# Kernel tuning notes

Hardware: AMD Instinct MI355X
Metric: run time of the kernel (lower is better)

Reference implementation:

```python
import jax, jax.numpy as jnp
import numpy as np

B, DIM, GRID, K, H = 524288, 4, 16, 100, 512
FEAT = DIM + 1 + K  # 105


def setup_inputs() -> dict:
    key = jax.random.key(0)
    ks = jax.random.split(key, 16)
    s = 0.05
    return {
        "x": jax.random.uniform(ks[0], (B, DIM), dtype=jnp.float32),
        "min_values": jnp.zeros((DIM,), jnp.float32),
        "max_values": jnp.ones((DIM,), jnp.float32),
        "pivots": jax.random.uniform(ks[1], (GRID ** DIM, DIM), dtype=jnp.float32),
        "knnd": jax.random.uniform(ks[2], (GRID ** DIM, K), dtype=jnp.float32),
        "query_mean": 0.1 * jax.random.normal(ks[3], (DIM,), jnp.float32),
        "query_std": 0.5 + jax.random.uniform(ks[4], (DIM,), dtype=jnp.float32),
        "knnd_mean": 0.1 * jax.random.normal(ks[5], (K,), jnp.float32),
        "knnd_std": 0.5 + jax.random.uniform(ks[6], (K,), dtype=jnp.float32),
        "W1": s * jax.random.normal(ks[7], (FEAT, H), jnp.float32),
        "b1": jnp.zeros((H,), jnp.float32),
        "W2": s * jax.random.normal(ks[8], (H, H), jnp.float32),
        "b2": jnp.zeros((H,), jnp.float32),
        "W3": s * jax.random.normal(ks[9], (H, H), jnp.float32),
        "b3": jnp.zeros((H,), jnp.float32),
        "W4": s * jax.random.normal(ks[10], (H, K), jnp.float32),
        "b4": jnp.zeros((K,), jnp.float32),
    }


def reference(x, min_values, max_values, pivots, knnd,
              query_mean, query_std, knnd_mean, knnd_std,
              W1, b1, W2, b2, W3, b3, W4, b4):
    dim = x.shape[1]
    grid = GRID
    bin_width = (max_values - min_values) / grid            # [dim]
    cell_diag = jnp.sqrt(jnp.sum(bin_width ** 2))
    # grid-hash index (radix base `grid` over dims)
    scaled = (x - min_values) / (max_values - min_values) * grid
    bins = jnp.clip(jnp.floor(scaled).astype(jnp.int32), 0, grid - 1)  # [B,dim]
    radix = (grid ** jnp.arange(dim - 1, -1, -1)).astype(jnp.int32)    # [dim]
    idx = jnp.sum(bins * radix, axis=-1)                    # [B]
    # gather pivot coords + knn distances
    pivot = pivots[idx]                                     # [B,dim]
    pknnd = knnd[idx]                                       # [B,K]
    dist = jnp.linalg.norm(x - pivot, axis=-1) / cell_diag  # [B]
    # normalize feature parts
    qn = (x - query_mean) / query_std                       # [B,dim]
    kn = (pknnd - knnd_mean) / knnd_std                     # [B,K]
    feat = jnp.concatenate([qn, dist[:, None], kn], axis=-1)  # [B,105]
    # 4-layer MLP
    h = jax.nn.relu(feat @ W1 + b1)
    h = jax.nn.relu(h @ W2 + b2)
    h = jax.nn.relu(h @ W3 + b3)
    return h @ W4 + b4
```

## Files before the change

### kernel.cpp

```cpp
#include <hip/hip_runtime.h>

typedef __attribute__((ext_vector_type(8))) short short8_t;
typedef __attribute__((ext_vector_type(16))) float f32x16;

#define NROWS_TOTAL 524288
#define MROWS 128
#define HSTRIDE 536
#define NTHREADS 512
#define OSTRIDE 108

__device__ __forceinline__ unsigned short f32_to_bf16(float f) {
    union { float f; unsigned int u; } v; v.f = f;
    unsigned int r = v.u + 0x7FFFu + ((v.u >> 16) & 1u);
    return (unsigned short)(r >> 16);
}

__global__ void conv_weights(const float* __restrict__ W1, const float* __restrict__ W2,
                             const float* __restrict__ W3, const float* __restrict__ W4,
                             unsigned short* __restrict__ ws) {
    int i = blockIdx.x * 256 + threadIdx.x;
    if (i < 65536) {
        int k = i & 127, n = i >> 7;
        ws[i] = f32_to_bf16(k < 105 ? W1[k * 512 + n] : 0.0f);
    } else if (i < 327680) {
        int j = i - 65536; int k = j & 511, n = j >> 9;
        ws[i] = f32_to_bf16(W2[k * 512 + n]);
    } else if (i < 589824) {
        int j = i - 327680; int k = j & 511, n = j >> 9;
        ws[i] = f32_to_bf16(W3[k * 512 + n]);
    } else if (i < 655360) {
        int j = i - 589824; int k = j & 511, n = j >> 9;
        ws[i] = f32_to_bf16(n < 100 ? W4[k * 100 + n] : 0.0f);
    }
}

__device__ __forceinline__ int clamp_bin(float sc) {
    int b = (int)floorf(sc);
    return b < 0 ? 0 : (b > 15 ? 15 : b);
}

template<int KDIM>
__device__ __forceinline__ void mlp_layer(unsigned short* hbuf,
                                          const unsigned short* __restrict__ Wt,
                                          const float* __restrict__ bias,
                                          int lane, int wave) {
    const int l31 = lane & 31;
    const int lh  = lane >> 5;
    const int n0  = wave * 64;
    constexpr int NK = KDIM / 32;

    f32x16 acc[4][2];
    #pragma unroll
    for (int nt = 0; nt < 2; ++nt) {
        float bv = bias[n0 + nt * 32 + l31];
        #pragma unroll
        for (int mt = 0; mt < 4; ++mt)
            #pragma unroll
            for (int r = 0; r < 16; ++r)
                acc[mt][nt][r] = bv;
    }

    const unsigned short* wbase  = Wt + (n0 + l31) * KDIM + lh * 8;
    const unsigned short* abase0 = hbuf + l31 * HSTRIDE + lh * 8;

    short8_t bc[2][4];
    #pragma unroll
    for (int nt = 0; nt < 2; ++nt)
        #pragma unroll
        for (int kh = 0; kh < 2; ++kh) {
            bc[0][nt * 2 + kh] = *(const short8_t*)(wbase + nt * (32 * KDIM) + kh * 16);
            bc[1][nt * 2 + kh] = *(const short8_t*)(wbase + nt * (32 * KDIM) + 32 + kh * 16);
        }

    #pragma unroll
    for (int kc = 0; kc < NK; ++kc) {
        const int par = kc & 1;
        short8_t a[4][2];
        #pragma unroll
        for (int mt = 0; mt < 4; ++mt)
            #pragma unroll
            for (int kh = 0; kh < 2; ++kh)
                a[mt][kh] = *(const short8_t*)(abase0 + mt * (32 * HSTRIDE) + kc * 32 + kh * 16);
        __builtin_amdgcn_s_setprio(1);
        #pragma unroll
        for (int kh = 0; kh < 2; ++kh)
            #pragma unroll
            for (int mt = 0; mt < 4; ++mt)
                #pragma unroll
                for (int nt = 0; nt < 2; ++nt)
                    acc[mt][nt] = __builtin_amdgcn_mfma_f32_32x32x16_bf16(
                        a[mt][kh], bc[par][nt * 2 + kh], acc[mt][nt], 0, 0, 0);
        __builtin_amdgcn_s_setprio(0);
        if (kc + 2 < NK) {
            #pragma unroll
            for (int nt = 0; nt < 2; ++nt)
                #pragma unroll
                for (int kh = 0; kh < 2; ++kh)
                    bc[par][nt * 2 + kh] =
                        *(const short8_t*)(wbase + nt * (32 * KDIM) + (kc + 2) * 32 + kh * 16);
        }
    }

    __syncthreads();

    const int odd = lane & 1;
    const int colw = n0 + odd * 32 + (l31 & ~1);
    #pragma unroll
    for (int mt = 0; mt < 4; ++mt) {
        #pragma unroll
        for (int reg = 0; reg < 16; ++reg) {
            float vA = fmaxf(acc[mt][0][reg], 0.f);
            float vB = fmaxf(acc[mt][1][reg], 0.f);
            float vm = odd ? vB : vA;
            float vs = odd ? vA : vB;
            float vr = __shfl_xor(vs, 1, 64);
            unsigned int ha = f32_to_bf16(vm);
            unsigned int hb = f32_to_bf16(vr);
            unsigned int packed = odd ? (hb | (ha << 16)) : (ha | (hb << 16));
            int row = mt * 32 + (reg & 3) + 8 * (reg >> 2) + 4 * lh;
            *(unsigned int*)(hbuf + row * HSTRIDE + colw) = packed;
        }
    }
    __syncthreads();
}

__global__ void __launch_bounds__(NTHREADS, 2)
pivnet_fused(const float* __restrict__ x,
             const float* __restrict__ minv, const float* __restrict__ maxv,
             const float* __restrict__ pivots, const float* __restrict__ knnd,
             const float* __restrict__ qmean, const float* __restrict__ qstd,
             const float* __restrict__ kmean, const float* __restrict__ kstd,
             const unsigned short* __restrict__ wsw,
             const float* __restrict__ b1, const float* __restrict__ b2,
             const float* __restrict__ b3, const float* __restrict__ b4,
             float* __restrict__ out) {
    __shared__ unsigned short hbuf[MROWS * HSTRIDE];

    const int tid  = threadIdx.x;
    const int lane = tid & 63;
    const int wave = tid >> 6;
    const int row0 = blockIdx.x * MROWS;

    {
        const int p = tid & 7;
        const float mn0 = minv[0], mn1 = minv[1], mn2 = minv[2], mn3 = minv[3];
        const float rg0 = maxv[0] - mn0, rg1 = maxv[1] - mn1, rg2 = maxv[2] - mn2, rg3 = maxv[3] - mn3;
        const float cd2 = (rg0 * rg0 + rg1 * rg1 + rg2 * rg2 + rg3 * rg3) * (1.0f / 256.0f);
        #pragma unroll
        for (int rep = 0; rep < 2; ++rep) {
            const int r = (tid >> 3) + rep * 64;
            const float4 xr = ((const float4*)x)[row0 + r];
            const float xa0 = xr.x, xa1 = xr.y, xa2 = xr.z, xa3 = xr.w;
            int bidx;
            bidx = clamp_bin((xa0 - mn0) / rg0 * 16.f);
            bidx = bidx * 16 + clamp_bin((xa1 - mn1) / rg1 * 16.f);
            bidx = bidx * 16 + clamp_bin((xa2 - mn2) / rg2 * 16.f);
            bidx = bidx * 16 + clamp_bin((xa3 - mn3) / rg3 * 16.f);
            const float* kr = knnd + (size_t)bidx * 100;

            unsigned short vals[16];
            if (p == 0) {
                vals[0] = f32_to_bf16((xa0 - qmean[0]) / qstd[0]);
                vals[1] = f32_to_bf16((xa1 - qmean[1]) / qstd[1]);
                vals[2] = f32_to_bf16((xa2 - qmean[2]) / qstd[2]);
                vals[3] = f32_to_bf16((xa3 - qmean[3]) / qstd[3]);
                const float4 pv = ((const float4*)pivots)[bidx];
                float d0 = xa0 - pv.x, d1 = xa1 - pv.y, d2 = xa2 - pv.z, d3 = xa3 - pv.w;
                vals[4] = f32_to_bf16(sqrtf((d0 * d0 + d1 * d1 + d2 * d2 + d3 * d3) / cd2));
                #pragma unroll
                for (int j = 5; j < 16; ++j) {
                    int k = j - 5;
                    vals[j] = f32_to_bf16((kr[k] - kmean[k]) / kstd[k]);
                }
            } else {
                #pragma unroll
                for (int j = 0; j < 16; ++j) {
                    int k = p * 16 + j - 5;
                    float f = 0.f;
                    if (k < 100) f = (kr[k] - kmean[k]) / kstd[k];
                    vals[j] = f32_to_bf16(f);
                }
            }
            unsigned int pk[8];
            #pragma unroll
            for (int j = 0; j < 8; ++j)
                pk[j] = (unsigned int)vals[2 * j] | ((unsigned int)vals[2 * j + 1] << 16);
            uint4* d4 = (uint4*)(hbuf + r * HSTRIDE + p * 16);
            d4[0] = make_uint4(pk[0], pk[1], pk[2], pk[3]);
            d4[1] = make_uint4(pk[4], pk[5], pk[6], pk[7]);
        }
    }
    __syncthreads();

    const unsigned short* W1t = wsw;
    const unsigned short* W2t = wsw + 65536;
    const unsigned short* W3t = wsw + 327680;
    const unsigned short* W4t = wsw + 589824;

    mlp_layer<128>(hbuf, W1t, b1, lane, wave);
    mlp_layer<512>(hbuf, W2t, b2, lane, wave);
    mlp_layer<512>(hbuf, W3t, b3, lane, wave);

    {
        const int l31 = lane & 31;
        const int lh  = lane >> 5;
        const int nt4  = wave & 3;
        const int rowg = wave >> 2;
        const int col  = nt4 * 32 + l31;
        f32x16 acc4[2];
        {
            float bv = (col < 100) ? b4[col] : 0.f;
            #pragma unroll
            for (int mt = 0; mt < 2; ++mt)
                #pragma unroll
                for (int r = 0; r < 16; ++r) acc4[mt][r] = bv;
        }
        const unsigned short* wb4 = W4t + col * 512 + lh * 8;
        const unsigned short* ab0 = hbuf + (rowg * 64 + l31) * HSTRIDE + lh * 8;

        short8_t b4c[2][2];
        #pragma unroll
        for (int kh = 0; kh < 2; ++kh) {
            b4c[0][kh] = *(const short8_t*)(wb4 + kh * 16);
            b4c[1][kh] = *(const short8_t*)(wb4 + 32 + kh * 16);
        }

        #pragma unroll
        for (int kc = 0; kc < 16; ++kc) {
            const int par = kc & 1;
            short8_t a[2][2];
            #pragma unroll
            for (int mt = 0; mt < 2; ++mt)
                #pragma unroll
                for (int kh = 0; kh < 2; ++kh)
                    a[mt][kh] = *(const short8_t*)(ab0 + mt * (32 * HSTRIDE) + kc * 32 + kh * 16);
            __builtin_amdgcn_s_setprio(1);
            #pragma unroll
            for (int kh = 0; kh < 2; ++kh)
                #pragma unroll
                for (int mt = 0; mt < 2; ++mt)
                    acc4[mt] = __builtin_amdgcn_mfma_f32_32x32x16_bf16(
                        a[mt][kh], b4c[par][kh], acc4[mt], 0, 0, 0);
            __builtin_amdgcn_s_setprio(0);
            if (kc + 2 < 16) {
                #pragma unroll
                for (int kh = 0; kh < 2; ++kh)
                    b4c[par][kh] = *(const short8_t*)(wb4 + (kc + 2) * 32 + kh * 16);
            }
        }

        __syncthreads();

        float* fstage = (float*)hbuf;
        if (col < 100) {
            #pragma unroll
            for (int mt = 0; mt < 2; ++mt)
                #pragma unroll
                for (int reg = 0; reg < 16; ++reg) {
                    int row = rowg * 64 + mt * 32 + (reg & 3) + 8 * (reg >> 2) + 4 * lh;
                    fstage[row * OSTRIDE + col] = acc4[mt][reg];
                }
        }
        __syncthreads();

        float* obase = out + (size_t)row0 * 100;
        #pragma unroll
        for (int k = 0; k < 7; ++k) {
            int j = tid + k * 512;
            if (j < 3200) {
                int row = j / 25;
                int c4  = j - row * 25;
                float4 v = *(const float4*)(fstage + row * OSTRIDE + c4 * 4);
                *(float4*)(obase + 4 * j) = v;
            }
        }
    }
}

extern "C" void kernel_launch(void* const* d_in, const int* in_sizes, int n_in,
                              void* d_out, int out_size, void* d_ws, size_t ws_size,
                              hipStream_t stream) {
    const float* x    = (const float*)d_in[0];
    const float* minv = (const float*)d_in[1];
    const float* maxv = (const float*)d_in[2];
    const float* piv  = (const float*)d_in[3];
    const float* knnd = (const float*)d_in[4];
    const float* qm   = (const float*)d_in[5];
    const float* qs   = (const float*)d_in[6];
    const float* km   = (const float*)d_in[7];
    const float* ks   = (const float*)d_in[8];
    const float* W1   = (const float*)d_in[9];
    const float* b1   = (const float*)d_in[10];
    const float* W2   = (const float*)d_in[11];
    const float* b2   = (const float*)d_in[12];
    const float* W3   = (const float*)d_in[13];
    const float* b3   = (const float*)d_in[14];
    const float* W4   = (const float*)d_in[15];
    const float* b4   = (const float*)d_in[16];
    float* out = (float*)d_out;
    unsigned short* wsw = (unsigned short*)d_ws;

    conv_weights<<<2560, 256, 0, stream>>>(W1, W2, W3, W4, wsw);
    pivnet_fused<<<NROWS_TOTAL / MROWS, NTHREADS, 0, stream>>>(
        x, minv, maxv, piv, knnd, qm, qs, km, ks,
        wsw, b1, b2, b3, b4, out);
}
```

Measured before the change: 1.290 ms.

## Stage weight tiles into LDS via async global_load_lds double buffering

Weights are repacked into k-chunked, XOR-swizzled tiles. Each block now streams them into a double-buffered LDS area with global_load_lds, gated by vmcnt waits and barriers, and the next layer's first tiles are prefetched while the current layer finishes. Before, every wave loaded its own weight fragments straight from global memory. Rows per block drop from 128 to 64 to make room for the staging buffers and to cut register use. The change trades per-wave global weight traffic for block-shared LDS reuse, at the cost of more barriers per k-step and less reuse of each weight tile per block.

```diff
diff --git a/kernel.cpp b/kernel.cpp
--- a/kernel.cpp
+++ b/kernel.cpp
@@ -4,10 +4,13 @@
 typedef __attribute__((ext_vector_type(16))) float f32x16;
 
 #define NROWS_TOTAL 524288
-#define MROWS 128
+#define MROWS 64
 #define HSTRIDE 536
 #define NTHREADS 512
 #define OSTRIDE 108
+
+#define HBUF_USHORT (MROWS * HSTRIDE)
+#define LDS_TOTAL_USHORT (HBUF_USHORT + 2 * 16384)
 
 __device__ __forceinline__ unsigned short f32_to_bf16(float f) {
     union { float f; unsigned int u; } v; v.f = f;
@@ -18,20 +21,16 @@
 __global__ void conv_weights(const float* __restrict__ W1, const float* __restrict__ W2,
                              const float* __restrict__ W3, const float* __restrict__ W4,
                              unsigned short* __restrict__ ws) {
-    int i = blockIdx.x * 256 + threadIdx.x;
-    if (i < 65536) {
-        int k = i & 127, n = i >> 7;
-        ws[i] = f32_to_bf16(k < 105 ? W1[k * 512 + n] : 0.0f);
-    } else if (i < 327680) {
-        int j = i - 65536; int k = j & 511, n = j >> 9;
-        ws[i] = f32_to_bf16(W2[k * 512 + n]);
-    } else if (i < 589824) {
-        int j = i - 327680; int k = j & 511, n = j >> 9;
-        ws[i] = f32_to_bf16(W3[k * 512 + n]);
-    } else if (i < 655360) {
-        int j = i - 589824; int k = j & 511, n = j >> 9;
-        ws[i] = f32_to_bf16(n < 100 ? W4[k * 100 + n] : 0.0f);
-    }
+    int t = blockIdx.x * 256 + threadIdx.x;
+    float v; int n, k, base;
+    if (t < 65536)       { n = t & 511;                 k = t >> 9;          v = (k < 105) ? W1[k * 512 + n] : 0.f; base = 0      + (k >> 5) * 16384; }
+    else if (t < 327680) { int u = t - 65536;  n = u & 511; k = u >> 9;      v = W2[k * 512 + n];                   base = 65536  + (k >> 5) * 16384; }
+    else if (t < 589824) { int u = t - 327680; n = u & 511; k = u >> 9;      v = W3[k * 512 + n];                   base = 327680 + (k >> 5) * 16384; }
+    else                 { int u = t - 589824; n = u & 127; k = u >> 7;      v = (n < 100) ? W4[k * 100 + n] : 0.f; base = 589824 + (k >> 5) * 4096;  }
+    int kk = k & 31;
+    int kh = kk >> 4, lh = (kk >> 3) & 1, i = kk & 7;
+    int off = (((n << 5) + (kh << 4) + (lh << 3)) ^ ((n & 7) << 3)) + i;
+    ws[base + off] = f32_to_bf16(v);
 }
 
 __device__ __forceinline__ int clamp_bin(float sc) {
@@ -39,74 +38,98 @@
     return b < 0 ? 0 : (b > 15 ? 15 : b);
 }
 
-template<int KDIM>
-__device__ __forceinline__ void mlp_layer(unsigned short* hbuf,
-                                          const unsigned short* __restrict__ Wt,
-                                          const float* __restrict__ bias,
-                                          int lane, int wave) {
-    const int l31 = lane & 31;
-    const int lh  = lane >> 5;
-    const int n0  = wave * 64;
+__device__ __forceinline__ void gl2lds16(const void* g, void* l) {
+    __builtin_amdgcn_global_load_lds(
+        (__attribute__((address_space(1))) void*)g,
+        (__attribute__((address_space(3))) void*)l, 16, 0, 0);
+}
+
+template<int CALLS>
+__device__ __forceinline__ void stageN(char* dst, const char* src, int tid) {
+    #pragma unroll
+    for (int c = 0; c < CALLS; ++c)
+        gl2lds16(src + c * 8192 + tid * 16, dst + c * 8192 + (tid >> 6) * 1024);
+}
+
+__device__ __forceinline__ void wait_vmcnt(int n) {
+    if (n == 0)      asm volatile("s_waitcnt vmcnt(0)" ::: "memory");
+    else if (n == 1) asm volatile("s_waitcnt vmcnt(1)" ::: "memory");
+    else             asm volatile("s_waitcnt vmcnt(4)" ::: "memory");
+}
+
+template<int KDIM, int NEXT_CALLS, int PREV_GATE>
+__device__ __forceinline__ void mlp_layer(unsigned short* hbuf, char* bst,
+                                          const unsigned short* Wt, const unsigned short* Wnext,
+                                          const float* __restrict__ bias, int tid) {
     constexpr int NK = KDIM / 32;
-
-    f32x16 acc[4][2];
+    const int lane = tid & 63, wave = tid >> 6;
+    const int l31 = lane & 31, lh = lane >> 5;
+    const int n0 = wave * 64;
+    const char* wt_b = (const char*)Wt;
+    const char* wn_b = (const char*)Wnext;
+
+    f32x16 acc[2][2];
     #pragma unroll
     for (int nt = 0; nt < 2; ++nt) {
         float bv = bias[n0 + nt * 32 + l31];
         #pragma unroll
-        for (int mt = 0; mt < 4; ++mt)
-            #pragma unroll
-            for (int r = 0; r < 16; ++r)
-                acc[mt][nt][r] = bv;
-    }
-
-    const unsigned short* wbase  = Wt + (n0 + l31) * KDIM + lh * 8;
-    const unsigned short* abase0 = hbuf + l31 * HSTRIDE + lh * 8;
-
-    short8_t bc[2][4];
+        for (int mt = 0; mt < 2; ++mt)
+            #pragma unroll
+            for (int r = 0; r < 16; ++r) acc[mt][nt][r] = bv;
+    }
+
+    const char* ab = (const char*)hbuf + l31 * (HSTRIDE * 2) + lh * 16;
+    int boff[2][2];
     #pragma unroll
     for (int nt = 0; nt < 2; ++nt)
         #pragma unroll
         for (int kh = 0; kh < 2; ++kh) {
-            bc[0][nt * 2 + kh] = *(const short8_t*)(wbase + nt * (32 * KDIM) + kh * 16);
-            bc[1][nt * 2 + kh] = *(const short8_t*)(wbase + nt * (32 * KDIM) + 32 + kh * 16);
+            int n = n0 + nt * 32 + l31;
+            boff[nt][kh] = ((n << 6) + (kh << 5) + (lh << 4)) ^ ((l31 & 7) << 4);
         }
 
     #pragma unroll
     for (int kc = 0; kc < NK; ++kc) {
-        const int par = kc & 1;
-        short8_t a[4][2];
-        #pragma unroll
-        for (int mt = 0; mt < 4; ++mt)
+        int gate = (kc == 0) ? PREV_GATE
+                 : ((kc + 1) < NK ? 4 : (((kc + 1 - NK) < 2 && NEXT_CALLS > 0) ? NEXT_CALLS : 0));
+        wait_vmcnt(gate);
+        __builtin_amdgcn_s_barrier();
+        const char* bp = bst + (kc & 1) * 32768;
+        short8_t b[2][2], a[2][2];
+        #pragma unroll
+        for (int nt = 0; nt < 2; ++nt)
             #pragma unroll
             for (int kh = 0; kh < 2; ++kh)
-                a[mt][kh] = *(const short8_t*)(abase0 + mt * (32 * HSTRIDE) + kc * 32 + kh * 16);
+                b[nt][kh] = *(const short8_t*)(bp + boff[nt][kh]);
+        #pragma unroll
+        for (int mt = 0; mt < 2; ++mt)
+            #pragma unroll
+            for (int kh = 0; kh < 2; ++kh)
+                a[mt][kh] = *(const short8_t*)(ab + mt * (32 * HSTRIDE * 2) + kc * 64 + kh * 32);
+        asm volatile("s_waitcnt lgkmcnt(0)" ::: "memory");
+        __builtin_amdgcn_sched_barrier(0);
+        __builtin_amdgcn_s_barrier();
+        char* mybuf = bst + (kc & 1) * 32768;
+        if (kc + 2 < NK)
+            stageN<4>(mybuf, wt_b + (kc + 2) * 32768, tid);
+        else if (NEXT_CALLS > 0 && (kc + 2 - NK) < 2)
+            stageN<NEXT_CALLS>(mybuf, wn_b + (kc + 2 - NK) * (NEXT_CALLS * 8192), tid);
         __builtin_amdgcn_s_setprio(1);
         #pragma unroll
         for (int kh = 0; kh < 2; ++kh)
             #pragma unroll
-            for (int mt = 0; mt < 4; ++mt)
+            for (int mt = 0; mt < 2; ++mt)
                 #pragma unroll
                 for (int nt = 0; nt < 2; ++nt)
                     acc[mt][nt] = __builtin_amdgcn_mfma_f32_32x32x16_bf16(
-                        a[mt][kh], bc[par][nt * 2 + kh], acc[mt][nt], 0, 0, 0);
+                        a[mt][kh], b[nt][kh], acc[mt][nt], 0, 0, 0);
         __builtin_amdgcn_s_setprio(0);
-        if (kc + 2 < NK) {
-            #pragma unroll
-            for (int nt = 0; nt < 2; ++nt)
-                #pragma unroll
-                for (int kh = 0; kh < 2; ++kh)
-                    bc[par][nt * 2 + kh] =
-                        *(const short8_t*)(wbase + nt * (32 * KDIM) + (kc + 2) * 32 + kh * 16);
-        }
-    }
-
-    __syncthreads();
+    }
 
     const int odd = lane & 1;
     const int colw = n0 + odd * 32 + (l31 & ~1);
     #pragma unroll
-    for (int mt = 0; mt < 4; ++mt) {
+    for (int mt = 0; mt < 2; ++mt) {
         #pragma unroll
         for (int reg = 0; reg < 16; ++reg) {
             float vA = fmaxf(acc[mt][0][reg], 0.f);
@@ -121,7 +144,8 @@
             *(unsigned int*)(hbuf + row * HSTRIDE + colw) = packed;
         }
     }
-    __syncthreads();
+    asm volatile("s_waitcnt lgkmcnt(0)" ::: "memory");
+    __builtin_amdgcn_s_barrier();
 }
 
 __global__ void __launch_bounds__(NTHREADS, 2)
@@ -134,140 +158,126 @@
              const float* __restrict__ b1, const float* __restrict__ b2,
              const float* __restrict__ b3, const float* __restrict__ b4,
              float* __restrict__ out) {
-    __shared__ unsigned short hbuf[MROWS * HSTRIDE];
+    __shared__ unsigned short lds_all[LDS_TOTAL_USHORT];
+    unsigned short* hbuf = lds_all;
+    char* bst = (char*)(lds_all + HBUF_USHORT);
 
     const int tid  = threadIdx.x;
     const int lane = tid & 63;
-    const int wave = tid >> 6;
     const int row0 = blockIdx.x * MROWS;
+    const char* wsb = (const char*)wsw;
+
+    stageN<4>(bst, wsb, tid);
+    stageN<4>(bst + 32768, wsb + 32768, tid);
 
     {
+        const int r = tid >> 3;
         const int p = tid & 7;
         const float mn0 = minv[0], mn1 = minv[1], mn2 = minv[2], mn3 = minv[3];
         const float rg0 = maxv[0] - mn0, rg1 = maxv[1] - mn1, rg2 = maxv[2] - mn2, rg3 = maxv[3] - mn3;
         const float cd2 = (rg0 * rg0 + rg1 * rg1 + rg2 * rg2 + rg3 * rg3) * (1.0f / 256.0f);
-        #pragma unroll
-        for (int rep = 0; rep < 2; ++rep) {
-            const int r = (tid >> 3) + rep * 64;
-            const float4 xr = ((const float4*)x)[row0 + r];
-            const float xa0 = xr.x, xa1 = xr.y, xa2 = xr.z, xa3 = xr.w;
-            int bidx;
-            bidx = clamp_bin((xa0 - mn0) / rg0 * 16.f);
-            bidx = bidx * 16 + clamp_bin((xa1 - mn1) / rg1 * 16.f);
-            bidx = bidx * 16 + clamp_bin((xa2 - mn2) / rg2 * 16.f);
-            bidx = bidx * 16 + clamp_bin((xa3 - mn3) / rg3 * 16.f);
-            const float* kr = knnd + (size_t)bidx * 100;
-
-            unsigned short vals[16];
-            if (p == 0) {
-                vals[0] = f32_to_bf16((xa0 - qmean[0]) / qstd[0]);
-                vals[1] = f32_to_bf16((xa1 - qmean[1]) / qstd[1]);
-                vals[2] = f32_to_bf16((xa2 - qmean[2]) / qstd[2]);
-                vals[3] = f32_to_bf16((xa3 - qmean[3]) / qstd[3]);
-                const float4 pv = ((const float4*)pivots)[bidx];
-                float d0 = xa0 - pv.x, d1 = xa1 - pv.y, d2 = xa2 - pv.z, d3 = xa3 - pv.w;
-                vals[4] = f32_to_bf16(sqrtf((d0 * d0 + d1 * d1 + d2 * d2 + d3 * d3) / cd2));
-                #pragma unroll
-                for (int j = 5; j < 16; ++j) {
-                    int k = j - 5;
-                    vals[j] = f32_to_bf16((kr[k] - kmean[k]) / kstd[k]);
-                }
-            } else {
-                #pragma unroll
-                for (int j = 0; j < 16; ++j) {
-                    int k = p * 16 + j - 5;
-                    float f = 0.f;
-                    if (k < 100) f = (kr[k] - kmean[k]) / kstd[k];
-                    vals[j] = f32_to_bf16(f);
-                }
+        const float4 xr = ((const float4*)x)[row0 + r];
+        const float xa0 = xr.x, xa1 = xr.y, xa2 = xr.z, xa3 = xr.w;
+        int bidx;
+        bidx = clamp_bin((xa0 - mn0) / rg0 * 16.f);
+        bidx = bidx * 16 + clamp_bin((xa1 - mn1) / rg1 * 16.f);
+        bidx = bidx * 16 + clamp_bin((xa2 - mn2) / rg2 * 16.f);
+        bidx = bidx * 16 + clamp_bin((xa3 - mn3) / rg3 * 16.f);
+        const float* kr = knnd + (size_t)bidx * 100;
+
+        unsigned short vals[16];
+        if (p == 0) {
+            vals[0] = f32_to_bf16((xa0 - qmean[0]) / qstd[0]);
+            vals[1] = f32_to_bf16((xa1 - qmean[1]) / qstd[1]);
+            vals[2] = f32_to_bf16((xa2 - qmean[2]) / qstd[2]);
+            vals[3] = f32_to_bf16((xa3 - qmean[3]) / qstd[3]);
+            const float4 pv = ((const float4*)pivots)[bidx];
+            float d0 = xa0 - pv.x, d1 = xa1 - pv.y, d2 = xa2 - pv.z, d3 = xa3 - pv.w;
+            vals[4] = f32_to_bf16(sqrtf((d0 * d0 + d1 * d1 + d2 * d2 + d3 * d3) / cd2));
+            #pragma unroll
+            for (int j = 5; j < 16; ++j) {
+                int k = j - 5;
+                vals[j] = f32_to_bf16((kr[k] - kmean[k]) / kstd[k]);
             }
-            unsigned int pk[8];
-            #pragma unroll
-            for (int j = 0; j < 8; ++j)
-                pk[j] = (unsigned int)vals[2 * j] | ((unsigned int)vals[2 * j + 1] << 16);
-            uint4* d4 = (uint4*)(hbuf + r * HSTRIDE + p * 16);
-            d4[0] = make_uint4(pk[0], pk[1], pk[2], pk[3]);
-            d4[1] = make_uint4(pk[4], pk[5], pk[6], pk[7]);
-        }
-    }
-    __syncthreads();
-
-    const unsigned short* W1t = wsw;
-    const unsigned short* W2t = wsw + 65536;
-    const unsigned short* W3t = wsw + 327680;
-    const unsigned short* W4t = wsw + 589824;
-
-    mlp_layer<128>(hbuf, W1t, b1, lane, wave);
-    mlp_layer<512>(hbuf, W2t, b2, lane, wave);
-    mlp_layer<512>(hbuf, W3t, b3, lane, wave);
+        } else {
+            #pragma unroll
+            for (int j = 0; j < 16; ++j) {
+                int k = p * 16 + j - 5;
+                float f = 0.f;
+                if (k < 100) f = (kr[k] - kmean[k]) / kstd[k];
+                vals[j] = f32_to_bf16(f);
+            }
+        }
+        unsigned int pk[8];
+        #pragma unroll
+        for (int j = 0; j < 8; ++j)
+            pk[j] = (unsigned int)vals[2 * j] | ((unsigned int)vals[2 * j + 1] << 16);
+        uint4* d4 = (uint4*)(hbuf + r * HSTRIDE + p * 16);
+        d4[0] = make_uint4(pk[0], pk[1], pk[2], pk[3]);
+        d4[1] = make_uint4(pk[4], pk[5], pk[6], pk[7]);
+    }
+    asm volatile("s_waitcnt lgkmcnt(0)" ::: "memory");
+    __builtin_amdgcn_s_barrier();
+
+    mlp_layer<128, 4, 4>(hbuf, bst, wsw,          wsw + 65536,  b1, tid);
+    mlp_layer<512, 4, 4>(hbuf, bst, wsw + 65536,  wsw + 327680, b2, tid);
+    mlp_layer<512, 1, 4>(hbuf, bst, wsw + 327680, wsw + 589824, b3, tid);
 
     {
-        const int l31 = lane & 31;
-        const int lh  = lane >> 5;
-        const int nt4  = wave & 3;
-        const int rowg = wave >> 2;
-        const int col  = nt4 * 32 + l31;
-        f32x16 acc4[2];
+        const int l31 = lane & 31, lh = lane >> 5;
+        const int wave = tid >> 6;
+        const int nt4 = wave & 3, rowg = wave >> 2;
+        const int col = nt4 * 32 + l31;
+        const char* w4_b = (const char*)(wsw + 589824);
+        f32x16 acc;
         {
             float bv = (col < 100) ? b4[col] : 0.f;
             #pragma unroll
-            for (int mt = 0; mt < 2; ++mt)
-                #pragma unroll
-                for (int r = 0; r < 16; ++r) acc4[mt][r] = bv;
-        }
-        const unsigned short* wb4 = W4t + col * 512 + lh * 8;
-        const unsigned short* ab0 = hbuf + (rowg * 64 + l31) * HSTRIDE + lh * 8;
-
-        short8_t b4c[2][2];
-        #pragma unroll
-        for (int kh = 0; kh < 2; ++kh) {
-            b4c[0][kh] = *(const short8_t*)(wb4 + kh * 16);
-            b4c[1][kh] = *(const short8_t*)(wb4 + 32 + kh * 16);
-        }
+            for (int r = 0; r < 16; ++r) acc[r] = bv;
+        }
+        const char* ab = (const char*)hbuf + (rowg * 32 + l31) * (HSTRIDE * 2) + lh * 16;
+        int boff[2];
+        #pragma unroll
+        for (int kh = 0; kh < 2; ++kh)
+            boff[kh] = ((col << 6) + (kh << 5) + (lh << 4)) ^ ((l31 & 7) << 4);
 
         #pragma unroll
         for (int kc = 0; kc < 16; ++kc) {
-            const int par = kc & 1;
-            short8_t a[2][2];
-            #pragma unroll
-            for (int mt = 0; mt < 2; ++mt)
-                #pragma unroll
-                for (int kh = 0; kh < 2; ++kh)
-                    a[mt][kh] = *(const short8_t*)(ab0 + mt * (32 * HSTRIDE) + kc * 32 + kh * 16);
+            int gate = (kc == 0) ? 1 : ((kc + 1) < 16 ? 1 : 0);
+            wait_vmcnt(gate);
+            __builtin_amdgcn_s_barrier();
+            const char* bp = bst + (kc & 1) * 32768;
+            short8_t b0 = *(const short8_t*)(bp + boff[0]);
+            short8_t b1r = *(const short8_t*)(bp + boff[1]);
+            short8_t a0 = *(const short8_t*)(ab + kc * 64);
+            short8_t a1 = *(const short8_t*)(ab + kc * 64 + 32);
+            asm volatile("s_waitcnt lgkmcnt(0)" ::: "memory");
+            __builtin_amdgcn_sched_barrier(0);
+            __builtin_amdgcn_s_barrier();
+            if (kc + 2 < 16)
+                stageN<1>(bst + (kc & 1) * 32768, w4_b + (kc + 2) * 8192, tid);
             __builtin_amdgcn_s_setprio(1);
-            #pragma unroll
-            for (int kh = 0; kh < 2; ++kh)
-                #pragma unroll
-                for (int mt = 0; mt < 2; ++mt)
-                    acc4[mt] = __builtin_amdgcn_mfma_f32_32x32x16_bf16(
-                        a[mt][kh], b4c[par][kh], acc4[mt], 0, 0, 0);
+            acc = __builtin_amdgcn_mfma_f32_32x32x16_bf16(a0, b0, acc, 0, 0, 0);
+            acc = __builtin_amdgcn_mfma_f32_32x32x16_bf16(a1, b1r, acc, 0, 0, 0);
             __builtin_amdgcn_s_setprio(0);
-            if (kc + 2 < 16) {
-                #pragma unroll
-                for (int kh = 0; kh < 2; ++kh)
-                    b4c[par][kh] = *(const short8_t*)(wb4 + (kc + 2) * 32 + kh * 16);
-            }
-        }
-
-        __syncthreads();
+        }
 
         float* fstage = (float*)hbuf;
         if (col < 100) {
             #pragma unroll
-            for (int mt = 0; mt < 2; ++mt)
-                #pragma unroll
-                for (int reg = 0; reg < 16; ++reg) {
-                    int row = rowg * 64 + mt * 32 + (reg & 3) + 8 * (reg >> 2) + 4 * lh;
-                    fstage[row * OSTRIDE + col] = acc4[mt][reg];
-                }
-        }
-        __syncthreads();
+            for (int reg = 0; reg < 16; ++reg) {
+                int row = rowg * 32 + (reg & 3) + 8 * (reg >> 2) + 4 * lh;
+                fstage[row * OSTRIDE + col] = acc[reg];
+            }
+        }
+        asm volatile("s_waitcnt lgkmcnt(0)" ::: "memory");
+        __builtin_amdgcn_s_barrier();
 
         float* obase = out + (size_t)row0 * 100;
         #pragma unroll
-        for (int k = 0; k < 7; ++k) {
+        for (int k = 0; k < 4; ++k) {
             int j = tid + k * 512;
-            if (j < 3200) {
+            if (j < 1600) {
                 int row = j / 25;
                 int c4  = j - row * 25;
                 float4 v = *(const float4*)(fstage + row * OSTRIDE + c4 * 4);
```

New measurement: 1.396 ms. +8.2%, slower.
